# Optimization experiments

Hardware: AMD Instinct MI355X
Metric: run time of the kernel (lower is better)

The kernel has to match this reference:

```python
import jax, jax.numpy as jnp
import numpy as np

EPS = 1e-8


def setup_inputs() -> dict:
    key = jax.random.key(0)
    ks = jax.random.split(key, 6)
    N, H, B = 1000000, 256, 1024
    x = jax.random.normal(ks[0], (N, H), dtype=jnp.float32)
    W1 = jax.random.normal(ks[1], (H, H // 2), dtype=jnp.float32) * (1.0 / np.sqrt(H))
    b1 = jax.random.normal(ks[2], (H // 2,), dtype=jnp.float32) * 0.01
    W2 = jax.random.normal(ks[3], (H // 2, 1), dtype=jnp.float32) * (1.0 / np.sqrt(H // 2))
    b2 = jax.random.normal(ks[4], (1,), dtype=jnp.float32) * 0.01
    batch = jnp.sort(jax.random.randint(ks[5], (N,), 0, B, dtype=jnp.int64))
    return {"x": x, "W1": W1, "b1": b1, "W2": W2, "b2": b2,
            "batch": batch, "batch_size": B}


def reference(x, W1, b1, W2, b2, batch, batch_size):
    # attention MLP: Linear -> Tanh -> Linear -> softmax over all nodes (dim 0)
    scores = jnp.tanh(x @ W1 + b1) @ W2 + b2          # [N, 1]
    w = jax.nn.softmax(scores, axis=0)[:, 0]           # [N]
    # per-graph normalization (segment sums replace the dense one-hot mask)
    seg_sum = jax.ops.segment_sum(w, batch, num_segments=batch_size)  # [B]
    w_norm = w / (seg_sum[batch] + EPS)                # [N]
    # weighted per-graph feature aggregation
    graph_embedding = jax.ops.segment_sum(w_norm[:, None] * x, batch,
                                          num_segments=batch_size)   # [B, H]
    return graph_embedding
```

## Files before the change

### kernel.cpp

```cpp
#include <hip/hip_runtime.h>
#include <hip/hip_bf16.h>
#include <cstdint>


#define H_DIM 256
#define HID   128

typedef _Float16 half8 __attribute__((ext_vector_type(8)));
typedef float floatx4 __attribute__((ext_vector_type(4)));

__device__ __forceinline__ float fast_tanh(float y) {
    float e2 = __expf(2.0f * y);
    return 1.0f - 2.0f / (e2 + 1.0f);
}

__global__ void prep_w1(const float* __restrict__ W1, _Float16* __restrict__ w1h) {
    int idx = blockIdx.x * blockDim.x + threadIdx.x;
    if (idx >= 8 * 8 * 64 * 8) return;
    int j  = idx & 7;
    int l  = (idx >> 3) & 63;
    int ks = (idx >> 9) & 7;
    int nt = idx >> 12;
    int k = ks * 32 + ((l >> 4) << 3) + j;
    int n = nt * 16 + (l & 15);
    w1h[idx] = (_Float16)W1[k * HID + n];
}

__global__ __launch_bounds__(512, 2) void score_kernel(
    const float* __restrict__ x, const _Float16* __restrict__ w1h,
    const float* __restrict__ b1, const float* __restrict__ W2,
    const float* __restrict__ b2, float* __restrict__ sout, int N)
{
    __shared__ __align__(16) _Float16 w1s[32768];
    int tid = threadIdx.x;
    {
        const uint4* src = (const uint4*)w1h;
        uint4* dst = (uint4*)w1s;
#pragma unroll
        for (int i = 0; i < 8; ++i) dst[tid + i * 512] = src[tid + i * 512];
    }
    __syncthreads();

    int wave = tid >> 6, lane = tid & 63;
    int g = lane >> 4, c = lane & 15;
    int node_base = blockIdx.x * 256 + wave * 32;

    int row0 = node_base + c;
    int row1 = row0 + 16;
    if (row0 > N - 1) row0 = N - 1;
    if (row1 > N - 1) row1 = N - 1;
    const float* xr0 = x + (size_t)row0 * H_DIM;
    const float* xr1 = x + (size_t)row1 * H_DIM;

    floatx4 acc[2][8];
#pragma unroll
    for (int mt = 0; mt < 2; ++mt)
#pragma unroll
        for (int nt = 0; nt < 8; ++nt)
#pragma unroll
            for (int q = 0; q < 4; ++q) acc[mt][nt][q] = 0.0f;

#pragma unroll
    for (int ks = 0; ks < 8; ++ks) {
        int kb = ks * 32 + g * 8;
        float4 a0 = *(const float4*)(xr0 + kb);
        float4 a1 = *(const float4*)(xr0 + kb + 4);
        float4 a2 = *(const float4*)(xr1 + kb);
        float4 a3 = *(const float4*)(xr1 + kb + 4);
        half8 af0, af1;
        af0[0] = (_Float16)a0.x; af0[1] = (_Float16)a0.y;
        af0[2] = (_Float16)a0.z; af0[3] = (_Float16)a0.w;
        af0[4] = (_Float16)a1.x; af0[5] = (_Float16)a1.y;
        af0[6] = (_Float16)a1.z; af0[7] = (_Float16)a1.w;
        af1[0] = (_Float16)a2.x; af1[1] = (_Float16)a2.y;
        af1[2] = (_Float16)a2.z; af1[3] = (_Float16)a2.w;
        af1[4] = (_Float16)a3.x; af1[5] = (_Float16)a3.y;
        af1[6] = (_Float16)a3.z; af1[7] = (_Float16)a3.w;
#pragma unroll
        for (int nt = 0; nt < 8; ++nt) {
            half8 bf = *(const half8*)&w1s[((nt * 8 + ks) * 64 + lane) * 8];
            acc[0][nt] = __builtin_amdgcn_mfma_f32_16x16x32_f16(af0, bf, acc[0][nt], 0, 0, 0);
            acc[1][nt] = __builtin_amdgcn_mfma_f32_16x16x32_f16(af1, bf, acc[1][nt], 0, 0, 0);
        }
    }

    float b1r[8], w2r[8];
#pragma unroll
    for (int nt = 0; nt < 8; ++nt) {
        b1r[nt] = b1[nt * 16 + c];
        w2r[nt] = W2[nt * 16 + c];
    }
    float b2v = b2[0];

#pragma unroll
    for (int mt = 0; mt < 2; ++mt) {
#pragma unroll
        for (int r = 0; r < 4; ++r) {
            float p = 0.0f;
#pragma unroll
            for (int nt = 0; nt < 8; ++nt)
                p += fast_tanh(acc[mt][nt][r] + b1r[nt]) * w2r[nt];
            p += __shfl_xor(p, 8);
            p += __shfl_xor(p, 4);
            p += __shfl_xor(p, 2);
            p += __shfl_xor(p, 1);
            if (c == 0) {
                int node = node_base + mt * 16 + g * 4 + r;
                if (node < N) sout[node] = p + b2v;
            }
        }
    }
}

__global__ __launch_bounds__(256) void pool_kernel(
    const float* __restrict__ x, const float* __restrict__ s,
    const int* __restrict__ batch, float* __restrict__ out, int N, int B)
{
    int b = blockIdx.x;
    int tid = threadIdx.x;

    int lo = 0, hi = N;
    while (lo < hi) { int mid = (lo + hi) >> 1; if (batch[mid] < b) lo = mid + 1; else hi = mid; }
    int start = lo;
    hi = N;
    while (lo < hi) { int mid = (lo + hi) >> 1; if (batch[mid] < b + 1) lo = mid + 1; else hi = mid; }
    int end = lo;

    if (start >= end) { out[(size_t)b * H_DIM + tid] = 0.0f; return; }

    __shared__ float red[4];
    __shared__ float bval[2];
    __shared__ float wl[256];
    int wid = tid >> 6, lane = tid & 63;

    float lm = -3.0e38f;
    for (int i = start + tid; i < end; i += 256) lm = fmaxf(lm, s[i]);
#pragma unroll
    for (int off = 32; off; off >>= 1) lm = fmaxf(lm, __shfl_xor(lm, off));
    if (lane == 0) red[wid] = lm;
    __syncthreads();
    if (tid == 0) bval[0] = fmaxf(fmaxf(red[0], red[1]), fmaxf(red[2], red[3]));
    __syncthreads();
    float m = bval[0];

    float lz = 0.0f;
    for (int i = start + tid; i < end; i += 256) lz += __expf(s[i] - m);
#pragma unroll
    for (int off = 32; off; off >>= 1) lz += __shfl_xor(lz, off);
    if (lane == 0) red[wid] = lz;
    __syncthreads();
    if (tid == 0) bval[1] = red[0] + red[1] + red[2] + red[3];
    __syncthreads();
    float Zinv = 1.0f / bval[1];

    float acc = 0.0f;
    for (int base = start; base < end; base += 256) {
        __syncthreads();
        int i = base + tid;
        wl[tid] = (i < end) ? __expf(s[i] - m) : 0.0f;
        __syncthreads();
        int cnt = min(256, end - base);
        const float* xp = x + (size_t)base * H_DIM + tid;
        for (int j = 0; j < cnt; ++j)
            acc = fmaf(wl[j], xp[(size_t)j * H_DIM], acc);
    }
    out[(size_t)b * H_DIM + tid] = acc * Zinv;
}

extern "C" void kernel_launch(void* const* d_in, const int* in_sizes, int n_in,
                              void* d_out, int out_size, void* d_ws, size_t ws_size,
                              hipStream_t stream) {
    const float* x   = (const float*)d_in[0];
    const float* W1  = (const float*)d_in[1];
    const float* b1  = (const float*)d_in[2];
    const float* W2  = (const float*)d_in[3];
    const float* b2  = (const float*)d_in[4];
    const int*  batch = (const int*)d_in[5];
    int N = in_sizes[5];
    int B = out_size / H_DIM;

    float* s = (float*)d_ws;
    size_t soff = (((size_t)N * sizeof(float)) + 255) & ~(size_t)255;
    _Float16* w1h = (_Float16*)((char*)d_ws + soff);

    prep_w1<<<32768 / 256, 256, 0, stream>>>(W1, w1h);

    int nblk = (N + 255) / 256;
    score_kernel<<<nblk, 512, 0, stream>>>(x, w1h, b1, W2, b2, s, N);

    pool_kernel<<<B, 256, 0, stream>>>(x, s, batch, (float*)d_out, N, B);
}
```

Baseline: 445.9 us.

## Fuse scoring MLP and segment pooling into one per-graph kernel with online softmax

Result: faster. 373.8 us (-16.2%).

```diff
diff --git a/kernel.cpp b/kernel.cpp
--- a/kernel.cpp
+++ b/kernel.cpp
@@ -5,6 +5,7 @@
 
 #define H_DIM 256
 #define HID   128
+#define CHUNK 64
 
 typedef _Float16 half8 __attribute__((ext_vector_type(8)));
 typedef float floatx4 __attribute__((ext_vector_type(4)));
@@ -26,167 +27,144 @@
     w1h[idx] = (_Float16)W1[k * HID + n];
 }
 
-__global__ __launch_bounds__(512, 2) void score_kernel(
+__global__ __launch_bounds__(256, 2) void fused_kernel(
     const float* __restrict__ x, const _Float16* __restrict__ w1h,
     const float* __restrict__ b1, const float* __restrict__ W2,
-    const float* __restrict__ b2, float* __restrict__ sout, int N)
+    const float* __restrict__ b2, const int* __restrict__ batch,
+    float* __restrict__ out, int N)
 {
     __shared__ __align__(16) _Float16 w1s[32768];
+    __shared__ float sbuf[CHUNK];
+    __shared__ float wbuf[CHUNK];
+    __shared__ float fstate;
+    __shared__ float zstate;
+
     int tid = threadIdx.x;
+    int b = blockIdx.x;
+
     {
         const uint4* src = (const uint4*)w1h;
         uint4* dst = (uint4*)w1s;
 #pragma unroll
-        for (int i = 0; i < 8; ++i) dst[tid + i * 512] = src[tid + i * 512];
+        for (int i = 0; i < 16; ++i) dst[tid + i * 256] = src[tid + i * 256];
     }
+
+    int lo = 0, hi = N;
+    while (lo < hi) { int mid = (lo + hi) >> 1; if (batch[mid] < b) lo = mid + 1; else hi = mid; }
+    int start = lo; hi = N;
+    while (lo < hi) { int mid = (lo + hi) >> 1; if (batch[mid] <= b) lo = mid + 1; else hi = mid; }
+    int end = lo;
+    int seglen = end - start;
+
+    if (seglen <= 0) { out[(size_t)b * H_DIM + tid] = 0.0f; return; }
+
     __syncthreads();
 
     int wave = tid >> 6, lane = tid & 63;
     int g = lane >> 4, c = lane & 15;
-    int node_base = blockIdx.x * 256 + wave * 32;
 
-    int row0 = node_base + c;
-    int row1 = row0 + 16;
-    if (row0 > N - 1) row0 = N - 1;
-    if (row1 > N - 1) row1 = N - 1;
-    const float* xr0 = x + (size_t)row0 * H_DIM;
-    const float* xr1 = x + (size_t)row1 * H_DIM;
+    float b1r[8], w2r[8];
+#pragma unroll
+    for (int nt = 0; nt < 8; ++nt) { b1r[nt] = b1[nt * 16 + c]; w2r[nt] = W2[nt * 16 + c]; }
+    float b2v = b2[0];
 
-    floatx4 acc[2][8];
-#pragma unroll
-    for (int mt = 0; mt < 2; ++mt)
+    float m_run = -3.0e38f;
+    float Zrun  = 0.0f;
+    float accv  = 0.0f;
+
+    for (int co = 0; co < seglen; co += CHUNK) {
+        int cnt = min(CHUNK, seglen - co);
+
+        int row = start + co + wave * 16 + c;
+        if (row > end - 1) row = end - 1;
+        const float* xr = x + (size_t)row * H_DIM;
+
+        floatx4 acc[8];
 #pragma unroll
         for (int nt = 0; nt < 8; ++nt)
 #pragma unroll
-            for (int q = 0; q < 4; ++q) acc[mt][nt][q] = 0.0f;
+            for (int q = 0; q < 4; ++q) acc[nt][q] = 0.0f;
 
 #pragma unroll
-    for (int ks = 0; ks < 8; ++ks) {
-        int kb = ks * 32 + g * 8;
-        float4 a0 = *(const float4*)(xr0 + kb);
-        float4 a1 = *(const float4*)(xr0 + kb + 4);
-        float4 a2 = *(const float4*)(xr1 + kb);
-        float4 a3 = *(const float4*)(xr1 + kb + 4);
-        half8 af0, af1;
-        af0[0] = (_Float16)a0.x; af0[1] = (_Float16)a0.y;
-        af0[2] = (_Float16)a0.z; af0[3] = (_Float16)a0.w;
-        af0[4] = (_Float16)a1.x; af0[5] = (_Float16)a1.y;
-        af0[6] = (_Float16)a1.z; af0[7] = (_Float16)a1.w;
-        af1[0] = (_Float16)a2.x; af1[1] = (_Float16)a2.y;
-        af1[2] = (_Float16)a2.z; af1[3] = (_Float16)a2.w;
-        af1[4] = (_Float16)a3.x; af1[5] = (_Float16)a3.y;
-        af1[6] = (_Float16)a3.z; af1[7] = (_Float16)a3.w;
+        for (int ks = 0; ks < 8; ++ks) {
+            int kb = ks * 32 + g * 8;
+            float4 a0 = *(const float4*)(xr + kb);
+            float4 a1 = *(const float4*)(xr + kb + 4);
+            half8 af;
+            af[0] = (_Float16)a0.x; af[1] = (_Float16)a0.y;
+            af[2] = (_Float16)a0.z; af[3] = (_Float16)a0.w;
+            af[4] = (_Float16)a1.x; af[5] = (_Float16)a1.y;
+            af[6] = (_Float16)a1.z; af[7] = (_Float16)a1.w;
 #pragma unroll
-        for (int nt = 0; nt < 8; ++nt) {
-            half8 bf = *(const half8*)&w1s[((nt * 8 + ks) * 64 + lane) * 8];
-            acc[0][nt] = __builtin_amdgcn_mfma_f32_16x16x32_f16(af0, bf, acc[0][nt], 0, 0, 0);
-            acc[1][nt] = __builtin_amdgcn_mfma_f32_16x16x32_f16(af1, bf, acc[1][nt], 0, 0, 0);
+            for (int nt = 0; nt < 8; ++nt) {
+                half8 bf = *(const half8*)&w1s[((nt * 8 + ks) * 64 + lane) * 8];
+                acc[nt] = __builtin_amdgcn_mfma_f32_16x16x32_f16(af, bf, acc[nt], 0, 0, 0);
+            }
         }
-    }
 
-    float b1r[8], w2r[8];
-#pragma unroll
-    for (int nt = 0; nt < 8; ++nt) {
-        b1r[nt] = b1[nt * 16 + c];
-        w2r[nt] = W2[nt * 16 + c];
-    }
-    float b2v = b2[0];
-
-#pragma unroll
-    for (int mt = 0; mt < 2; ++mt) {
 #pragma unroll
         for (int r = 0; r < 4; ++r) {
             float p = 0.0f;
 #pragma unroll
             for (int nt = 0; nt < 8; ++nt)
-                p += fast_tanh(acc[mt][nt][r] + b1r[nt]) * w2r[nt];
+                p += fast_tanh(acc[nt][r] + b1r[nt]) * w2r[nt];
             p += __shfl_xor(p, 8);
             p += __shfl_xor(p, 4);
             p += __shfl_xor(p, 2);
             p += __shfl_xor(p, 1);
             if (c == 0) {
-                int node = node_base + mt * 16 + g * 4 + r;
-                if (node < N) sout[node] = p + b2v;
+                int nl = wave * 16 + g * 4 + r;
+                sbuf[nl] = (nl < cnt) ? (p + b2v) : -3.0e38f;
             }
         }
+        __syncthreads();
+
+        if (wave == 0) {
+            float sv = sbuf[lane];
+            float cm = sv;
+#pragma unroll
+            for (int off = 32; off; off >>= 1) cm = fmaxf(cm, __shfl_xor(cm, off));
+            float m_new = fmaxf(m_run, cm);
+            float f = __expf(m_run - m_new);
+            float w = __expf(sv - m_new);
+            wbuf[lane] = w;
+            float sw = w;
+#pragma unroll
+            for (int off = 32; off; off >>= 1) sw += __shfl_xor(sw, off);
+            Zrun = Zrun * f + sw;
+            m_run = m_new;
+            if (lane == 0) fstate = f;
+        }
+        __syncthreads();
+
+        float f = fstate;
+        const float* xc = x + (size_t)(start + co) * H_DIM + tid;
+        float a = 0.0f;
+#pragma unroll 8
+        for (int j = 0; j < cnt; ++j)
+            a = fmaf(wbuf[j], xc[(size_t)j * H_DIM], a);
+        accv = accv * f + a;
     }
-}
 
-__global__ __launch_bounds__(256) void pool_kernel(
-    const float* __restrict__ x, const float* __restrict__ s,
-    const int* __restrict__ batch, float* __restrict__ out, int N, int B)
-{
-    int b = blockIdx.x;
-    int tid = threadIdx.x;
-
-    int lo = 0, hi = N;
-    while (lo < hi) { int mid = (lo + hi) >> 1; if (batch[mid] < b) lo = mid + 1; else hi = mid; }
-    int start = lo;
-    hi = N;
-    while (lo < hi) { int mid = (lo + hi) >> 1; if (batch[mid] < b + 1) lo = mid + 1; else hi = mid; }
-    int end = lo;
-
-    if (start >= end) { out[(size_t)b * H_DIM + tid] = 0.0f; return; }
-
-    __shared__ float red[4];
-    __shared__ float bval[2];
-    __shared__ float wl[256];
-    int wid = tid >> 6, lane = tid & 63;
-
-    float lm = -3.0e38f;
-    for (int i = start + tid; i < end; i += 256) lm = fmaxf(lm, s[i]);
-#pragma unroll
-    for (int off = 32; off; off >>= 1) lm = fmaxf(lm, __shfl_xor(lm, off));
-    if (lane == 0) red[wid] = lm;
+    if (tid == 0) zstate = Zrun;
     __syncthreads();
-    if (tid == 0) bval[0] = fmaxf(fmaxf(red[0], red[1]), fmaxf(red[2], red[3]));
-    __syncthreads();
-    float m = bval[0];
-
-    float lz = 0.0f;
-    for (int i = start + tid; i < end; i += 256) lz += __expf(s[i] - m);
-#pragma unroll
-    for (int off = 32; off; off >>= 1) lz += __shfl_xor(lz, off);
-    if (lane == 0) red[wid] = lz;
-    __syncthreads();
-    if (tid == 0) bval[1] = red[0] + red[1] + red[2] + red[3];
-    __syncthreads();
-    float Zinv = 1.0f / bval[1];
-
-    float acc = 0.0f;
-    for (int base = start; base < end; base += 256) {
-        __syncthreads();
-        int i = base + tid;
-        wl[tid] = (i < end) ? __expf(s[i] - m) : 0.0f;
-        __syncthreads();
-        int cnt = min(256, end - base);
-        const float* xp = x + (size_t)base * H_DIM + tid;
-        for (int j = 0; j < cnt; ++j)
-            acc = fmaf(wl[j], xp[(size_t)j * H_DIM], acc);
-    }
-    out[(size_t)b * H_DIM + tid] = acc * Zinv;
+    out[(size_t)b * H_DIM + tid] = accv / zstate;
 }
 
 extern "C" void kernel_launch(void* const* d_in, const int* in_sizes, int n_in,
                               void* d_out, int out_size, void* d_ws, size_t ws_size,
                               hipStream_t stream) {
-    const float* x   = (const float*)d_in[0];
-    const float* W1  = (const float*)d_in[1];
-    const float* b1  = (const float*)d_in[2];
-    const float* W2  = (const float*)d_in[3];
-    const float* b2  = (const float*)d_in[4];
-    const int*  batch = (const int*)d_in[5];
+    const float* x    = (const float*)d_in[0];
+    const float* W1   = (const float*)d_in[1];
+    const float* b1   = (const float*)d_in[2];
+    const float* W2   = (const float*)d_in[3];
+    const float* b2   = (const float*)d_in[4];
+    const int*   batch = (const int*)d_in[5];
     int N = in_sizes[5];
     int B = out_size / H_DIM;
 
-    float* s = (float*)d_ws;
-    size_t soff = (((size_t)N * sizeof(float)) + 255) & ~(size_t)255;
-    _Float16* w1h = (_Float16*)((char*)d_ws + soff);
+    _Float16* w1h = (_Float16*)d_ws;
 
     prep_w1<<<32768 / 256, 256, 0, stream>>>(W1, w1h);
-
-    int nblk = (N + 255) / 256;
-    score_kernel<<<nblk, 512, 0, stream>>>(x, w1h, b1, W2, b2, s, N);
-
-    pool_kernel<<<B, 256, 0, stream>>>(x, s, batch, (float*)d_out, N, B);
+    fused_kernel<<<B, 256, 0, stream>>>(x, w1h, b1, W2, b2, batch, (float*)d_out, N);
 }
```
